# Kernel tuning notes

Hardware: AMD Instinct MI355X
Metric: run time of the kernel (lower is better)

The kernel has to match this reference:

```python
import jax, jax.numpy as jnp
import numpy as np

B, N, HID, HEADS = 4, 512, 64, 4
D = HID // HEADS          # head_dim = 16
E_DIM = 1
SCALE = 1.0 / np.sqrt(D)
LN_EPS = 1e-5
NEG = -1e9


def _linear_init(k, fan_in, fan_out):
    lim = 1.0 / np.sqrt(fan_in)
    kw, kb = jax.random.split(k)
    W = jax.random.uniform(kw, (fan_in, fan_out), jnp.float32, -lim, lim)
    b = jax.random.uniform(kb, (fan_out,), jnp.float32, -lim, lim)
    return W, b


def setup_inputs() -> dict:
    key = jax.random.key(0)
    ks = jax.random.split(key, 8)
    W1_w, W1_b = _linear_init(ks[3], HID, HID)
    W2_w, W2_b = _linear_init(ks[4], HID, HID)
    W3_w, W3_b = _linear_init(ks[5], HID, HID)
    W4_w, W4_b = _linear_init(ks[6], HID, HID)
    W5_w, W5_b = _linear_init(ks[7], E_DIM, HID)
    return {
        "x": jax.random.normal(ks[0], (B, N, HID), jnp.float32),
        "adj": jax.random.randint(ks[1], (B, N, N), 0, 2, jnp.int32),
        "edge_features": jax.random.normal(ks[2], (B, N, N, E_DIM), jnp.float32),
        "W1_w": W1_w, "W1_b": W1_b,
        "W2_w": W2_w, "W2_b": W2_b,
        "W3_w": W3_w, "W3_b": W3_b,
        "W4_w": W4_w, "W4_b": W4_b,
        "W5_w": W5_w, "W5_b": W5_b,
        "ln_g": jnp.ones((HID,), jnp.float32),
        "ln_b": jnp.zeros((HID,), jnp.float32),
    }


def _layer_norm(y, g, b):
    m = jnp.mean(y, axis=-1, keepdims=True)
    v = jnp.mean(jnp.square(y - m), axis=-1, keepdims=True)
    return (y - m) * jax.lax.rsqrt(v + LN_EPS) * g + b


def reference(x, adj, edge_features, W1_w, W1_b, W2_w, W2_b, W3_w, W3_b,
              W4_w, W4_b, W5_w, W5_b, ln_g, ln_b):
    b, n, h = x.shape
    self_t = x @ W1_w + W1_b                               # [B,N,HID]
    Q = (x @ W3_w + W3_b).reshape(b, n, HEADS, D)          # [B,N,H,D]
    K = (x @ W4_w + W4_b).reshape(b, n, HEADS, D)          # [B,N,H,D]
    # edge contribution: W5 e_ij -> [B,N,N,H,D] (the big intermediate)
    Ec = (edge_features @ W5_w + W5_b).reshape(b, n, n, HEADS, D)
    # (Q_i . (K_j + E_ij)) split into node-pair GEMM + edge broadcast term
    scores = (jnp.einsum('bihd,bjhd->bhij', Q, K)
              + jnp.einsum('bihd,bijhd->bhij', Q, Ec)) * SCALE  # [B,H,N,N]
    scores = jnp.where(adj[:, None, :, :] == 0, NEG, scores)
    attn = jax.nn.softmax(scores, axis=-1)                 # dropout = identity (eval)
    V = (x @ W2_w + W2_b).reshape(b, n, HEADS, D)          # [B,N,H,D]
    msg = jnp.einsum('bhij,bjhd->bihd', attn, V).reshape(b, n, h)
    return _layer_norm(x + self_t + msg, ln_g, ln_b)
```

## Files before the change

### kernel.cpp

```cpp
#include <hip/hip_runtime.h>

#define B 4
#define N 512
#define HID 64
#define HEADS 4
#define DH 16
#define SCALE 0.25f
#define NEG (-1e9f)
#define LN_EPS 1e-5f

constexpr int ROWS = B * N;
constexpr size_t OFF_ST  = 0;
constexpr size_t OFF_Q   = (size_t)ROWS * HID;
constexpr size_t OFF_K   = 2 * OFF_Q;
constexpr size_t OFF_V   = 3 * OFF_Q;
constexpr size_t OFF_PART= 4 * OFF_Q;

__global__ __launch_bounds__(256) void proj_kernel(
    const float* __restrict__ x,
    const float* __restrict__ W1w, const float* __restrict__ W1b,
    const float* __restrict__ W2w, const float* __restrict__ W2b,
    const float* __restrict__ W3w, const float* __restrict__ W3b,
    const float* __restrict__ W4w, const float* __restrict__ W4b,
    float* __restrict__ ws)
{
  __shared__ float xsT[64 * 8];
  const int t = threadIdx.x;
  const int rows0 = blockIdx.x * 8;

  if (t < 128) {
    const float4 v = *(const float4*)&x[(size_t)rows0 * HID + t * 4];
    const int r = t >> 4;
    const int k0 = (t & 15) * 4;
    xsT[(k0 + 0) * 8 + r] = v.x;
    xsT[(k0 + 1) * 8 + r] = v.y;
    xsT[(k0 + 2) * 8 + r] = v.z;
    xsT[(k0 + 3) * 8 + r] = v.w;
  }
  __syncthreads();

  const int m = t >> 6;
  const int c = t & 63;
  const float* Ww; const float* Wb; size_t off;
  if      (m == 0) { Ww = W1w; Wb = W1b; off = OFF_ST; }
  else if (m == 1) { Ww = W3w; Wb = W3b; off = OFF_Q;  }
  else if (m == 2) { Ww = W4w; Wb = W4b; off = OFF_K;  }
  else             { Ww = W2w; Wb = W2b; off = OFF_V;  }

  float acc[8];
#pragma unroll
  for (int r = 0; r < 8; ++r) acc[r] = 0.f;

#pragma unroll 16
  for (int k = 0; k < 64; ++k) {
    const float w = Ww[(k << 6) + c];
    const float* xr = &xsT[k * 8];
    const float4 a0 = *(const float4*)(xr);
    const float4 a1 = *(const float4*)(xr + 4);
    acc[0] = fmaf(a0.x, w, acc[0]); acc[1] = fmaf(a0.y, w, acc[1]);
    acc[2] = fmaf(a0.z, w, acc[2]); acc[3] = fmaf(a0.w, w, acc[3]);
    acc[4] = fmaf(a1.x, w, acc[4]); acc[5] = fmaf(a1.y, w, acc[5]);
    acc[6] = fmaf(a1.z, w, acc[6]); acc[7] = fmaf(a1.w, w, acc[7]);
  }

  const float bias = Wb[c];
  const size_t base = off + (size_t)rows0 * HID + c;
#pragma unroll
  for (int r = 0; r < 8; ++r)
    ws[base + (size_t)r * HID] = acc[r] + bias;
}

__global__ __launch_bounds__(256, 4) void attn_kernel(
    const int*   __restrict__ adj,
    const float* __restrict__ efeat,
    const float* __restrict__ W5w, const float* __restrict__ W5b,
    float* __restrict__ ws)
{
  __shared__ float Ksh[256 * 20];
  __shared__ float Vsh[256 * 20];

  const int it = blockIdx.x, h = blockIdx.y;
  const int b    = blockIdx.z >> 1;
  const int half = blockIdx.z & 1;
  const int j0   = half << 8;
  const int t = threadIdx.x;
  const int g  = t & 15;
  const int il = t >> 4;
  const int i  = it * 16 + il;

  const float* Qb = ws + OFF_Q;
  const float* Kb = ws + OFF_K;
  const float* Vb = ws + OFF_V;
  float* part = ws + OFF_PART;

  {
    const int sj = t >> 2;
    const int dq = (t & 3) << 2;
#pragma unroll
    for (int p = 0; p < 4; ++p) {
      const int j = sj + (p << 6);
      const size_t gb = ((size_t)(b * N + j0 + j)) * HID + h * DH + dq;
      *(float4*)&Ksh[j * 20 + dq] = *(const float4*)&Kb[gb];
      *(float4*)&Vsh[j * 20 + dq] = *(const float4*)&Vb[gb];
    }
  }

  const float* qrow = Qb + ((size_t)(b * N + i)) * HID + h * DH;
  const float4 q0 = *(const float4*)(qrow);
  const float4 q1 = *(const float4*)(qrow + 4);
  const float4 q2 = *(const float4*)(qrow + 8);
  const float4 q3 = *(const float4*)(qrow + 12);
  const float4 w50 = *(const float4*)&W5w[h * DH];
  const float4 w51 = *(const float4*)&W5w[h * DH + 4];
  const float4 w52 = *(const float4*)&W5w[h * DH + 8];
  const float4 w53 = *(const float4*)&W5w[h * DH + 12];
  const float4 b50 = *(const float4*)&W5b[h * DH];
  const float4 b51 = *(const float4*)&W5b[h * DH + 4];
  const float4 b52 = *(const float4*)&W5b[h * DH + 8];
  const float4 b53 = *(const float4*)&W5b[h * DH + 12];
  const float qw5 = q0.x*w50.x + q0.y*w50.y + q0.z*w50.z + q0.w*w50.w
                  + q1.x*w51.x + q1.y*w51.y + q1.z*w51.z + q1.w*w51.w
                  + q2.x*w52.x + q2.y*w52.y + q2.z*w52.z + q2.w*w52.w
                  + q3.x*w53.x + q3.y*w53.y + q3.z*w53.z + q3.w*w53.w;
  const float qb5 = q0.x*b50.x + q0.y*b50.y + q0.z*b50.z + q0.w*b50.w
                  + q1.x*b51.x + q1.y*b51.y + q1.z*b51.z + q1.w*b51.w
                  + q2.x*b52.x + q2.y*b52.y + q2.z*b52.z + q2.w*b52.w
                  + q3.x*b53.x + q3.y*b53.y + q3.z*b53.z + q3.w*b53.w;

  __syncthreads();

  const int*   adjRow = adj   + ((size_t)(b * N + i)) * N + j0;
  const float* eRow   = efeat + ((size_t)(b * N + i)) * N + j0;

  float s[16];
#pragma unroll
  for (int jj = 0; jj < 16; ++jj) {
    const int j = g + (jj << 4);
    const int   a  = adjRow[j];
    const float ev = eRow[j];
    const float* kr = &Ksh[j * 20];
    const float4 k0 = *(const float4*)(kr);
    const float4 k1 = *(const float4*)(kr + 4);
    const float4 k2 = *(const float4*)(kr + 8);
    const float4 k3 = *(const float4*)(kr + 12);
    float sA = q0.x*k0.x, sB = q0.y*k0.y, sC = q0.z*k0.z, sD = q0.w*k0.w;
    sA = fmaf(q1.x,k1.x,sA); sB = fmaf(q1.y,k1.y,sB);
    sC = fmaf(q1.z,k1.z,sC); sD = fmaf(q1.w,k1.w,sD);
    sA = fmaf(q2.x,k2.x,sA); sB = fmaf(q2.y,k2.y,sB);
    sC = fmaf(q2.z,k2.z,sC); sD = fmaf(q2.w,k2.w,sD);
    sA = fmaf(q3.x,k3.x,sA); sB = fmaf(q3.y,k3.y,sB);
    sC = fmaf(q3.z,k3.z,sC); sD = fmaf(q3.w,k3.w,sD);
    const float sc = ((sA + sB) + (sC + sD) + ev * qw5 + qb5) * SCALE;
    s[jj] = (a == 0) ? NEG : sc;
  }

  float r8[8], r4[4];
#pragma unroll
  for (int k = 0; k < 8; ++k) r8[k] = fmaxf(s[k], s[k + 8]);
#pragma unroll
  for (int k = 0; k < 4; ++k) r4[k] = fmaxf(r8[k], r8[k + 4]);
  float M = fmaxf(fmaxf(r4[0], r4[1]), fmaxf(r4[2], r4[3]));
#pragma unroll
  for (int o = 1; o < 16; o <<= 1) M = fmaxf(M, __shfl_xor(M, o, 16));

  float l0 = 0.f, l1 = 0.f;
  float acc[16];
#pragma unroll
  for (int d = 0; d < 16; ++d) acc[d] = 0.f;

#pragma unroll
  for (int jj = 0; jj < 16; ++jj) {
    const int j = g + (jj << 4);
    const float p = __expf(s[jj] - M);
    if (jj & 1) l1 += p; else l0 += p;
    const float* vr = &Vsh[j * 20];
    const float4 v0 = *(const float4*)(vr);
    const float4 v1 = *(const float4*)(vr + 4);
    const float4 v2 = *(const float4*)(vr + 8);
    const float4 v3 = *(const float4*)(vr + 12);
    acc[0]  = fmaf(p, v0.x, acc[0]);  acc[1]  = fmaf(p, v0.y, acc[1]);
    acc[2]  = fmaf(p, v0.z, acc[2]);  acc[3]  = fmaf(p, v0.w, acc[3]);
    acc[4]  = fmaf(p, v1.x, acc[4]);  acc[5]  = fmaf(p, v1.y, acc[5]);
    acc[6]  = fmaf(p, v1.z, acc[6]);  acc[7]  = fmaf(p, v1.w, acc[7]);
    acc[8]  = fmaf(p, v2.x, acc[8]);  acc[9]  = fmaf(p, v2.y, acc[9]);
    acc[10] = fmaf(p, v2.z, acc[10]); acc[11] = fmaf(p, v2.w, acc[11]);
    acc[12] = fmaf(p, v3.x, acc[12]); acc[13] = fmaf(p, v3.y, acc[13]);
    acc[14] = fmaf(p, v3.z, acc[14]); acc[15] = fmaf(p, v3.w, acc[15]);
  }

  float lw = l0 + l1;
#pragma unroll
  for (int o = 1; o < 16; o <<= 1) lw += __shfl_xor(lw, o, 16);

  __syncthreads();
  float* P = Ksh;
  const int prow = (il * 16 + g) * 20;
  *(float4*)&P[prow +  0] = make_float4(acc[0],  acc[1],  acc[2],  acc[3]);
  *(float4*)&P[prow +  4] = make_float4(acc[4],  acc[5],  acc[6],  acc[7]);
  *(float4*)&P[prow +  8] = make_float4(acc[8],  acc[9],  acc[10], acc[11]);
  *(float4*)&P[prow + 12] = make_float4(acc[12], acc[13], acc[14], acc[15]);
  __syncthreads();

  float ssum = 0.f;
#pragma unroll
  for (int gp = 0; gp < 16; ++gp)
    ssum += P[(il * 16 + gp) * 20 + g];

  float* rec = part + ((((size_t)(b * N + i)) * HEADS + h) * 2 + half) * 18;
  rec[g] = ssum;
  if (g == 0) { rec[16] = M; rec[17] = lw; }
}

__global__ __launch_bounds__(256) void ln_kernel(
    const float* __restrict__ x, const float* __restrict__ ws,
    const float* __restrict__ gamma, const float* __restrict__ beta,
    float* __restrict__ out)
{
  const int t = threadIdx.x;
  const int lane = t & 63;
  const int row = blockIdx.x * 4 + (t >> 6);
  const size_t idx = (size_t)row * HID + lane;
  const float* ST   = ws + OFF_ST;
  const float* part = ws + OFF_PART;

  const int h = lane >> 4;
  const int d = lane & 15;
  const float* rec0 = part + (((size_t)row * HEADS + h) * 2 + 0) * 18;
  const float* rec1 = rec0 + 18;
  const float a0 = rec0[d], m0 = rec0[16], e0 = rec0[17];
  const float a1 = rec1[d], m1 = rec1[16], e1 = rec1[17];
  const float M  = fmaxf(m0, m1);
  const float w0 = __expf(m0 - M), w1 = __expf(m1 - M);
  const float msg = (a0 * w0 + a1 * w1) / (e0 * w0 + e1 * w1);

  const float v = x[idx] + ST[idx] + msg;
  float mu = v;
#pragma unroll
  for (int o = 1; o < 64; o <<= 1) mu += __shfl_xor(mu, o, 64);
  mu *= (1.0f / 64.0f);
  const float dv = v - mu;
  float var = dv * dv;
#pragma unroll
  for (int o = 1; o < 64; o <<= 1) var += __shfl_xor(var, o, 64);
  var *= (1.0f / 64.0f);
  out[idx] = dv * rsqrtf(var + LN_EPS) * gamma[lane] + beta[lane];
}

extern "C" void kernel_launch(void* const* d_in, const int* in_sizes, int n_in,
                              void* d_out, int out_size, void* d_ws, size_t ws_size,
                              hipStream_t stream)
{
  const float* x   = (const float*)d_in[0];
  const int*   adj = (const int*)d_in[1];
  const float* ef  = (const float*)d_in[2];
  const float* W1w = (const float*)d_in[3];
  const float* W1b = (const float*)d_in[4];
  const float* W2w = (const float*)d_in[5];
  const float* W2b = (const float*)d_in[6];
  const float* W3w = (const float*)d_in[7];
  const float* W3b = (const float*)d_in[8];
  const float* W4w = (const float*)d_in[9];
  const float* W4b = (const float*)d_in[10];
  const float* W5w = (const float*)d_in[11];
  const float* W5b = (const float*)d_in[12];
  const float* lng = (const float*)d_in[13];
  const float* lnb = (const float*)d_in[14];
  float* ws  = (float*)d_ws;
  float* out = (float*)d_out;

  proj_kernel<<<ROWS / 8, 256, 0, stream>>>(x, W1w, W1b, W2w, W2b, W3w, W3b, W4w, W4b, ws);
  attn_kernel<<<dim3(32, HEADS, B * 2), 256, 0, stream>>>(adj, ef, W5w, W5b, ws);
  ln_kernel<<<ROWS / 4, 256, 0, stream>>>(x, ws, lng, lnb, out);
}
```

Measured before the change: 23.16 us.

## Vectorize adj/edge loads with early issue and halve rows per projection block

The attention kernel now reads adjacency and edge-feature rows as int4/float4 vectors at the start, before the K/V shared-memory staging, so the global latency overlaps the staging. K and V rows are stored in shared memory under a permuted row index so each thread's four consecutive j values map to strided shared rows. The projection kernel processes 4 rows per block instead of 8, doubling the grid to spread the small GEMM across more CUs. This costs extra register pressure from the preloaded vectors and more redundant weight reads in the projection.

```diff
diff --git a/kernel.cpp b/kernel.cpp
--- a/kernel.cpp
+++ b/kernel.cpp
@@ -24,18 +24,18 @@
     const float* __restrict__ W4w, const float* __restrict__ W4b,
     float* __restrict__ ws)
 {
-  __shared__ float xsT[64 * 8];
+  __shared__ float xsT[64 * 4];
   const int t = threadIdx.x;
-  const int rows0 = blockIdx.x * 8;
-
-  if (t < 128) {
+  const int rows0 = blockIdx.x * 4;
+
+  if (t < 64) {
     const float4 v = *(const float4*)&x[(size_t)rows0 * HID + t * 4];
     const int r = t >> 4;
     const int k0 = (t & 15) * 4;
-    xsT[(k0 + 0) * 8 + r] = v.x;
-    xsT[(k0 + 1) * 8 + r] = v.y;
-    xsT[(k0 + 2) * 8 + r] = v.z;
-    xsT[(k0 + 3) * 8 + r] = v.w;
+    xsT[(k0 + 0) * 4 + r] = v.x;
+    xsT[(k0 + 1) * 4 + r] = v.y;
+    xsT[(k0 + 2) * 4 + r] = v.z;
+    xsT[(k0 + 3) * 4 + r] = v.w;
   }
   __syncthreads();
 
@@ -47,26 +47,22 @@
   else if (m == 2) { Ww = W4w; Wb = W4b; off = OFF_K;  }
   else             { Ww = W2w; Wb = W2b; off = OFF_V;  }
 
-  float acc[8];
-#pragma unroll
-  for (int r = 0; r < 8; ++r) acc[r] = 0.f;
+  float acc[4];
+#pragma unroll
+  for (int r = 0; r < 4; ++r) acc[r] = 0.f;
 
 #pragma unroll 16
   for (int k = 0; k < 64; ++k) {
     const float w = Ww[(k << 6) + c];
-    const float* xr = &xsT[k * 8];
-    const float4 a0 = *(const float4*)(xr);
-    const float4 a1 = *(const float4*)(xr + 4);
+    const float4 a0 = *(const float4*)&xsT[k * 4];
     acc[0] = fmaf(a0.x, w, acc[0]); acc[1] = fmaf(a0.y, w, acc[1]);
     acc[2] = fmaf(a0.z, w, acc[2]); acc[3] = fmaf(a0.w, w, acc[3]);
-    acc[4] = fmaf(a1.x, w, acc[4]); acc[5] = fmaf(a1.y, w, acc[5]);
-    acc[6] = fmaf(a1.z, w, acc[6]); acc[7] = fmaf(a1.w, w, acc[7]);
   }
 
   const float bias = Wb[c];
   const size_t base = off + (size_t)rows0 * HID + c;
 #pragma unroll
-  for (int r = 0; r < 8; ++r)
+  for (int r = 0; r < 4; ++r)
     ws[base + (size_t)r * HID] = acc[r] + bias;
 }
 
@@ -93,15 +89,27 @@
   const float* Vb = ws + OFF_V;
   float* part = ws + OFF_PART;
 
+  const int*   adjRow = adj   + ((size_t)(b * N + i)) * N + j0;
+  const float* eRow   = efeat + ((size_t)(b * N + i)) * N + j0;
+  int4   av0 = *(const int4*)  &adjRow[4 * g];
+  int4   av1 = *(const int4*)  &adjRow[4 * g + 64];
+  int4   av2 = *(const int4*)  &adjRow[4 * g + 128];
+  int4   av3 = *(const int4*)  &adjRow[4 * g + 192];
+  float4 ev0 = *(const float4*)&eRow  [4 * g];
+  float4 ev1 = *(const float4*)&eRow  [4 * g + 64];
+  float4 ev2 = *(const float4*)&eRow  [4 * g + 128];
+  float4 ev3 = *(const float4*)&eRow  [4 * g + 192];
+
   {
     const int sj = t >> 2;
     const int dq = (t & 3) << 2;
 #pragma unroll
     for (int p = 0; p < 4; ++p) {
-      const int j = sj + (p << 6);
+      const int j  = sj + (p << 6);
+      const int sr = ((j & 3) << 6) | (j >> 2);
       const size_t gb = ((size_t)(b * N + j0 + j)) * HID + h * DH + dq;
-      *(float4*)&Ksh[j * 20 + dq] = *(const float4*)&Kb[gb];
-      *(float4*)&Vsh[j * 20 + dq] = *(const float4*)&Vb[gb];
+      *(float4*)&Ksh[sr * 20 + dq] = *(const float4*)&Kb[gb];
+      *(float4*)&Vsh[sr * 20 + dq] = *(const float4*)&Vb[gb];
     }
   }
 
@@ -129,29 +137,35 @@
 
   __syncthreads();
 
-  const int*   adjRow = adj   + ((size_t)(b * N + i)) * N + j0;
-  const float* eRow   = efeat + ((size_t)(b * N + i)) * N + j0;
-
   float s[16];
 #pragma unroll
-  for (int jj = 0; jj < 16; ++jj) {
-    const int j = g + (jj << 4);
-    const int   a  = adjRow[j];
-    const float ev = eRow[j];
-    const float* kr = &Ksh[j * 20];
-    const float4 k0 = *(const float4*)(kr);
-    const float4 k1 = *(const float4*)(kr + 4);
-    const float4 k2 = *(const float4*)(kr + 8);
-    const float4 k3 = *(const float4*)(kr + 12);
-    float sA = q0.x*k0.x, sB = q0.y*k0.y, sC = q0.z*k0.z, sD = q0.w*k0.w;
-    sA = fmaf(q1.x,k1.x,sA); sB = fmaf(q1.y,k1.y,sB);
-    sC = fmaf(q1.z,k1.z,sC); sD = fmaf(q1.w,k1.w,sD);
-    sA = fmaf(q2.x,k2.x,sA); sB = fmaf(q2.y,k2.y,sB);
-    sC = fmaf(q2.z,k2.z,sC); sD = fmaf(q2.w,k2.w,sD);
-    sA = fmaf(q3.x,k3.x,sA); sB = fmaf(q3.y,k3.y,sB);
-    sC = fmaf(q3.z,k3.z,sC); sD = fmaf(q3.w,k3.w,sD);
-    const float sc = ((sA + sB) + (sC + sD) + ev * qw5 + qb5) * SCALE;
-    s[jj] = (a == 0) ? NEG : sc;
+  for (int q = 0; q < 4; ++q) {
+#pragma unroll
+    for (int r = 0; r < 4; ++r) {
+      const int a    = (r == 0) ? (q==0?av0.x:q==1?av1.x:q==2?av2.x:av3.x)
+                     : (r == 1) ? (q==0?av0.y:q==1?av1.y:q==2?av2.y:av3.y)
+                     : (r == 2) ? (q==0?av0.z:q==1?av1.z:q==2?av2.z:av3.z)
+                                : (q==0?av0.w:q==1?av1.w:q==2?av2.w:av3.w);
+      const float ev = (r == 0) ? (q==0?ev0.x:q==1?ev1.x:q==2?ev2.x:ev3.x)
+                     : (r == 1) ? (q==0?ev0.y:q==1?ev1.y:q==2?ev2.y:ev3.y)
+                     : (r == 2) ? (q==0?ev0.z:q==1?ev1.z:q==2?ev2.z:ev3.z)
+                                : (q==0?ev0.w:q==1?ev1.w:q==2?ev2.w:ev3.w);
+      const int sr = (r << 6) | (g + (q << 4));
+      const float* kr = &Ksh[sr * 20];
+      const float4 k0 = *(const float4*)(kr);
+      const float4 k1 = *(const float4*)(kr + 4);
+      const float4 k2 = *(const float4*)(kr + 8);
+      const float4 k3 = *(const float4*)(kr + 12);
+      float sA = q0.x*k0.x, sB = q0.y*k0.y, sC = q0.z*k0.z, sD = q0.w*k0.w;
+      sA = fmaf(q1.x,k1.x,sA); sB = fmaf(q1.y,k1.y,sB);
+      sC = fmaf(q1.z,k1.z,sC); sD = fmaf(q1.w,k1.w,sD);
+      sA = fmaf(q2.x,k2.x,sA); sB = fmaf(q2.y,k2.y,sB);
+      sC = fmaf(q2.z,k2.z,sC); sD = fmaf(q2.w,k2.w,sD);
+      sA = fmaf(q3.x,k3.x,sA); sB = fmaf(q3.y,k3.y,sB);
+      sC = fmaf(q3.z,k3.z,sC); sD = fmaf(q3.w,k3.w,sD);
+      const float sc = ((sA + sB) + (sC + sD) + ev * qw5 + qb5) * SCALE;
+      s[(q << 2) | r] = (a == 0) ? NEG : sc;
+    }
   }
 
   float r8[8], r4[4];
@@ -169,23 +183,27 @@
   for (int d = 0; d < 16; ++d) acc[d] = 0.f;
 
 #pragma unroll
-  for (int jj = 0; jj < 16; ++jj) {
-    const int j = g + (jj << 4);
-    const float p = __expf(s[jj] - M);
-    if (jj & 1) l1 += p; else l0 += p;
-    const float* vr = &Vsh[j * 20];
-    const float4 v0 = *(const float4*)(vr);
-    const float4 v1 = *(const float4*)(vr + 4);
-    const float4 v2 = *(const float4*)(vr + 8);
-    const float4 v3 = *(const float4*)(vr + 12);
-    acc[0]  = fmaf(p, v0.x, acc[0]);  acc[1]  = fmaf(p, v0.y, acc[1]);
-    acc[2]  = fmaf(p, v0.z, acc[2]);  acc[3]  = fmaf(p, v0.w, acc[3]);
-    acc[4]  = fmaf(p, v1.x, acc[4]);  acc[5]  = fmaf(p, v1.y, acc[5]);
-    acc[6]  = fmaf(p, v1.z, acc[6]);  acc[7]  = fmaf(p, v1.w, acc[7]);
-    acc[8]  = fmaf(p, v2.x, acc[8]);  acc[9]  = fmaf(p, v2.y, acc[9]);
-    acc[10] = fmaf(p, v2.z, acc[10]); acc[11] = fmaf(p, v2.w, acc[11]);
-    acc[12] = fmaf(p, v3.x, acc[12]); acc[13] = fmaf(p, v3.y, acc[13]);
-    acc[14] = fmaf(p, v3.z, acc[14]); acc[15] = fmaf(p, v3.w, acc[15]);
+  for (int q = 0; q < 4; ++q) {
+#pragma unroll
+    for (int r = 0; r < 4; ++r) {
+      const int idx = (q << 2) | r;
+      const float p = __expf(s[idx] - M);
+      if (idx & 1) l1 += p; else l0 += p;
+      const int sr = (r << 6) | (g + (q << 4));
+      const float* vr = &Vsh[sr * 20];
+      const float4 v0 = *(const float4*)(vr);
+      const float4 v1 = *(const float4*)(vr + 4);
+      const float4 v2 = *(const float4*)(vr + 8);
+      const float4 v3 = *(const float4*)(vr + 12);
+      acc[0]  = fmaf(p, v0.x, acc[0]);  acc[1]  = fmaf(p, v0.y, acc[1]);
+      acc[2]  = fmaf(p, v0.z, acc[2]);  acc[3]  = fmaf(p, v0.w, acc[3]);
+      acc[4]  = fmaf(p, v1.x, acc[4]);  acc[5]  = fmaf(p, v1.y, acc[5]);
+      acc[6]  = fmaf(p, v1.z, acc[6]);  acc[7]  = fmaf(p, v1.w, acc[7]);
+      acc[8]  = fmaf(p, v2.x, acc[8]);  acc[9]  = fmaf(p, v2.y, acc[9]);
+      acc[10] = fmaf(p, v2.z, acc[10]); acc[11] = fmaf(p, v2.w, acc[11]);
+      acc[12] = fmaf(p, v3.x, acc[12]); acc[13] = fmaf(p, v3.y, acc[13]);
+      acc[14] = fmaf(p, v3.z, acc[14]); acc[15] = fmaf(p, v3.w, acc[15]);
+    }
   }
 
   float lw = l0 + l1;
@@ -268,7 +286,7 @@
   float* ws  = (float*)d_ws;
   float* out = (float*)d_out;
 
-  proj_kernel<<<ROWS / 8, 256, 0, stream>>>(x, W1w, W1b, W2w, W2b, W3w, W3b, W4w, W4b, ws);
+  proj_kernel<<<ROWS / 4, 256, 0, stream>>>(x, W1w, W1b, W2w, W2b, W3w, W3b, W4w, W4b, ws);
   attn_kernel<<<dim3(32, HEADS, B * 2), 256, 0, stream>>>(adj, ef, W5w, W5b, ws);
   ln_kernel<<<ROWS / 4, 256, 0, stream>>>(x, ws, lng, lnb, out);
 }
```

Result: no change. 23.04 us (-0.5%).
